# Performance work log

Measured on AMD Instinct MI355X. Metric: run time of the kernel, lower is better.

## Reference

```python
import jax, jax.numpy as jnp
import numpy as np

B, N, IN_F, E, H, A = 8, 1024, 1024, 256, 4, 64
ALPHA = 0.2          # leaky relu slope
NEG = -9e15          # mask value from original code


def setup_inputs() -> dict:
    key = jax.random.key(0)
    k = jax.random.split(key, 7)
    x = jax.random.normal(k[0], (B * N, IN_F), dtype=jnp.float32)
    adj = jax.random.randint(k[1], (B, N, N), 0, 2, dtype=jnp.int32)
    # per-head GAT params: W (H, IN_F, E); a split into a1, a2 (H, E) each,
    # since cat([Wh_i, Wh_j]) @ a == Wh_i @ a1 + Wh_j @ a2 exactly.
    W = jax.random.normal(k[2], (H, IN_F, E), dtype=jnp.float32) * 0.05
    a1 = jax.random.normal(k[3], (H, E), dtype=jnp.float32) * 0.05
    a2 = jax.random.normal(k[4], (H, E), dtype=jnp.float32) * 0.05
    W_act = jax.random.normal(k[5], (H * E, A), dtype=jnp.float32) * 0.05
    b_act = jnp.zeros((A,), dtype=jnp.float32)
    return {"x": x, "adj": adj, "W": W, "a1": a1, "a2": a2,
            "W_act": W_act, "b_act": b_act}


def reference(x, adj, W, a1, a2, W_act, b_act):
    b, n, _ = adj.shape
    xr = x.reshape(b, n, -1)                                   # (B, N, IN_F)
    Wh = jnp.einsum('bni,hio->hbno', xr, W)                    # (H, B, N, E)
    f1 = jnp.einsum('hbno,ho->hbn', Wh, a1)                    # a . Wh_i part
    f2 = jnp.einsum('hbno,ho->hbn', Wh, a2)                    # a . Wh_j part
    e = jax.nn.leaky_relu(f1[..., :, None] + f2[..., None, :], ALPHA)  # (H,B,N,N)
    e = jnp.where(adj[None] > 0, e, NEG)
    att = jax.nn.softmax(e, axis=-1)                           # masked softmax
    h_prime = jnp.einsum('hbnm,hbmo->hbno', att, Wh)           # (H, B, N, E)
    h_prime = jax.nn.elu(h_prime)                              # concat=True -> elu
    feat = jnp.transpose(h_prime, (1, 2, 0, 3)).reshape(b * n, H * E)
    return feat @ W_act + b_act                                # (B*N, A)
```

## Files before the change

### kernel.cpp

```cpp
#include <hip/hip_runtime.h>
#include <stdint.h>

typedef __attribute__((ext_vector_type(8))) short short8;
typedef __attribute__((ext_vector_type(4))) float f32x4;
typedef __attribute__((ext_vector_type(16))) float f32x16;


__device__ __forceinline__ float b2f(unsigned short u) {
    union { unsigned int i; float f; } v; v.i = ((unsigned int)u) << 16; return v.f;
}
__device__ __forceinline__ unsigned short f2b(float f) {
    union { float f; unsigned int i; } v; v.f = f;
    unsigned int u = v.i;
    u = (u + 0x7FFFu + ((u >> 16) & 1u)) >> 16;
    return (unsigned short)u;
}
__device__ __forceinline__ unsigned int cvtpk(float a, float b) {
    unsigned int r;
    asm("v_cvt_pk_bf16_f32 %0, %1, %2" : "=v"(r) : "v"(a), "v"(b));
    return r;
}
__device__ __forceinline__ float blo(unsigned int u) {
    union { unsigned int i; float f; } v; v.i = u << 16; return v.f;
}
__device__ __forceinline__ float bhi(unsigned int u) {
    union { unsigned int i; float f; } v; v.i = u & 0xFFFF0000u; return v.f;
}
__device__ __forceinline__ void glds16(const void* g, const void* l) {
    __builtin_amdgcn_global_load_lds(
        (const __attribute__((address_space(1))) unsigned int*)g,
        (__attribute__((address_space(3))) unsigned int*)l, 16, 0, 0);
}

__device__ __forceinline__ void cvt8(const void* in, unsigned short* out,
                                     int f, int grp) {
    if (f) {
        ((ushort4*)out)[grp * 2]     = ((const ushort4*)in)[grp * 2];
        ((ushort4*)out)[grp * 2 + 1] = ((const ushort4*)in)[grp * 2 + 1];
    } else {
        const float4* p = (const float4*)in + (size_t)grp * 2;
        float4 a = p[0], b = p[1];
        ushort4 o0, o1;
        o0.x = f2b(a.x); o0.y = f2b(a.y); o0.z = f2b(a.z); o0.w = f2b(a.w);
        o1.x = f2b(b.x); o1.y = f2b(b.y); o1.z = f2b(b.z); o1.w = f2b(b.w);
        ((ushort4*)out)[grp * 2]     = o0;
        ((ushort4*)out)[grp * 2 + 1] = o1;
    }
}

__global__ __launch_bounds__(256) void prep_all(
        const unsigned int* __restrict__ x4,
        const void* __restrict__ x, const void* __restrict__ W,
        const void* __restrict__ Wact,
        const void* __restrict__ a1, const void* __restrict__ a2,
        const void* __restrict__ bact,
        unsigned short* __restrict__ xb, unsigned short* __restrict__ WT,
        unsigned short* __restrict__ WactT,
        unsigned short* __restrict__ a1b, unsigned short* __restrict__ a2b,
        unsigned short* __restrict__ bactb,
        int* __restrict__ flag, float4* __restrict__ fz) {
    __shared__ unsigned int tile[64 * 65];
    __shared__ int sflag;
    int tid = threadIdx.x;
    int bid = blockIdx.x;
    if (bid >= 4352 && bid < 4416) {
        fz[(bid - 4352) * 256 + tid] = float4{0.f, 0.f, 0.f, 0.f};
        return;
    }
    if (tid < 64) {
        unsigned int wv = x4[tid];
        unsigned int e = (wv >> 7) & 0xFF;
        unsigned long long m = __ballot(e >= 100 && e <= 140);
        if (tid == 0) sflag = (__popcll(m) >= 48) ? 1 : 0;
    }
    __syncthreads();
    int f = sflag;

    if (bid < 4096) {
        cvt8(x, xb, f, bid * 256 + tid);
        return;
    }
    if (bid == 4416) {
        if (tid == 0) flag[0] = f;
        if (tid < 128) cvt8(a1, a1b, f, tid);
        else           cvt8(a2, a2b, f, tid - 128);
        if (tid < 8)   cvt8(bact, bactb, f, tid);
        return;
    }
    const void* in; unsigned short* out; int C, bt, c0, r0;
    if (bid < 4352) {
        int lb = bid - 4096;
        in = W; out = WT; C = 256;
        c0 = (lb & 3) * 64;
        r0 = ((lb >> 2) & 15) * 64;
        bt = lb >> 6;
    } else {
        int lb = bid - 4417;
        in = Wact; out = WactT; C = 64;
        c0 = 0; r0 = lb * 64; bt = 0;
    }
    int rl = tid >> 2;
    int cc = (tid & 3) * 16;
    size_t ibase = ((size_t)bt * 1024 + (r0 + rl)) * C + c0 + cc;
    unsigned short v[16];
    if (f) {
        const unsigned short* p = (const unsigned short*)in + ibase;
        short8 a = *(const short8*)p;
        short8 b = *(const short8*)(p + 8);
#pragma unroll
        for (int j = 0; j < 8; j++) { v[j] = (unsigned short)a[j]; v[8 + j] = (unsigned short)b[j]; }
    } else {
        const float* p = (const float*)in + ibase;
#pragma unroll
        for (int j = 0; j < 16; j++) v[j] = f2b(p[j]);
    }
#pragma unroll
    for (int j = 0; j < 16; j++)
        tile[(cc + j) * 65 + rl] = v[j];
    __syncthreads();
    int cl = tid >> 2;
    int rch = (tid & 3) * 16;
    unsigned short o[16];
#pragma unroll
    for (int j = 0; j < 16; j++)
        o[j] = (unsigned short)tile[cl * 65 + rch + j];
    unsigned short* op = out + ((size_t)bt * C + (c0 + cl)) * 1024 + r0 + rch;
#pragma unroll
    for (int q = 0; q < 4; q++) {
        ushort4 s; s.x = o[q*4]; s.y = o[q*4+1]; s.z = o[q*4+2]; s.w = o[q*4+3];
        ((ushort4*)op)[q] = s;
    }
}

__global__ void pack_adj(const int* __restrict__ adj,
                         unsigned int* __restrict__ maskT) {
    int gid = blockIdx.x * 256 + threadIdx.x;
    int lane = threadIdx.x & 63;
    unsigned long long m = __ballot(adj[gid] > 0);
    if (lane == 0) {
        int lin = gid >> 6;
        int mw = (lin & 15) * 2;
        int bn = lin >> 4;
        int b = bn >> 10, n = bn & 1023;
        maskT[(size_t)(b * 32 + mw) * 1024 + n]     = (unsigned int)m;
        maskT[(size_t)(b * 32 + mw + 1) * 1024 + n] = (unsigned int)(m >> 32);
    }
}

__global__ __launch_bounds__(256) void k1_gemm(
        const unsigned short* __restrict__ x,
        const unsigned short* __restrict__ WT,
        unsigned short* __restrict__ WhF,
        const unsigned short* __restrict__ a1b,
        const unsigned short* __restrict__ a2b,
        float* __restrict__ f1, float* __restrict__ f2) {
    __shared__ unsigned short smA[2][16 * 512];
    __shared__ unsigned short smB[2][16 * 512];
    int tid = threadIdx.x;
    int w = tid >> 6, lane = tid & 63;
    int lr = lane & 15, lq = lane >> 4;
    int lin = blockIdx.x + 8 * blockIdx.y;
    int xcd = lin & 7, kk = lin >> 3;
    int ct = kk >> 3;
    int rt = xcd * 8 + (kk & 7);
    int col0 = ct * 128;
    int row0 = rt * 128;
    int h = col0 >> 8;
    int e_base = col0 & 255;
    int b = row0 >> 10;
    int m_base = row0 & 1023;
    int wr = w >> 1, wc = w & 1;

    f32x4 acc[4][4] = {};

    auto stage = [&](int bb, int k0) {
#pragma unroll
        for (int s = 0; s < 4; s++) {
            int g = 4 * w + s;
            int rb = g & 7, kh = g >> 3;
            const unsigned short* srcA =
                x + (size_t)(row0 + rb * 16 + lr) * 1024 + k0 + kh * 32 + lq * 8;
            glds16(srcA, &smA[bb][g * 512]);
            const unsigned short* srcB =
                WT + (size_t)(h * 256 + e_base + rb * 16 + lr) * 1024
                   + k0 + kh * 32 + lq * 8;
            glds16(srcB, &smB[bb][g * 512]);
        }
    };

    stage(0, 0);
    __syncthreads();

    for (int t = 0; t < 16; t++) {
        int cur = t & 1;
        if (t < 15) stage(cur ^ 1, (t + 1) * 64);
#pragma unroll
        for (int kh = 0; kh < 2; kh++) {
            short8 af[4], bf[4];
#pragma unroll
            for (int i = 0; i < 4; i++)
                af[i] = *(const short8*)&smA[cur][(kh * 8 + wr * 4 + i) * 512 + lane * 8];
#pragma unroll
            for (int j = 0; j < 4; j++)
                bf[j] = *(const short8*)&smB[cur][(kh * 8 + wc * 4 + j) * 512 + lane * 8];
#pragma unroll
            for (int i = 0; i < 4; i++)
#pragma unroll
                for (int j = 0; j < 4; j++)
                    acc[i][j] = __builtin_amdgcn_mfma_f32_16x16x32_bf16(
                        af[i], bf[j], acc[i][j], 0, 0, 0);
        }
        __syncthreads();
    }

    int hb = h * 8 + b;
#pragma unroll
    for (int i = 0; i < 4; i++) {
#pragma unroll
        for (int j = 0; j < 4; j++) {
            int e = e_base + (wc * 4 + j) * 16 + lr;
            int et = e >> 5, e31 = e & 31;
            int m16 = (m_base >> 4) + wr * 4 + i;
            ushort4 vs;
            vs.x = f2b(acc[i][j][0]);
            vs.y = f2b(acc[i][j][1]);
            vs.z = f2b(acc[i][j][2]);
            vs.w = f2b(acc[i][j][3]);
            size_t idx = ((size_t)((hb * 8 + et) * 64 + m16) * 512)
                         + ((lq >> 1) * 32 + e31) * 8 + (lq & 1) * 4;
            *(ushort4*)&WhF[idx] = vs;
        }
    }

    const float LOG2E = 1.44269504f;
    float a1v[4], a2v[4];
#pragma unroll
    for (int j = 0; j < 4; j++) {
        int e = e_base + (wc * 4 + j) * 16 + lr;
        a1v[j] = b2f(a1b[h * 256 + e]);
        a2v[j] = b2f(a2b[h * 256 + e]);
    }
#pragma unroll
    for (int i = 0; i < 4; i++) {
#pragma unroll
        for (int reg = 0; reg < 4; reg++) {
            float s1 = 0.f, s2 = 0.f;
#pragma unroll
            for (int j = 0; j < 4; j++) {
                s1 += acc[i][j][reg] * a1v[j];
                s2 += acc[i][j][reg] * a2v[j];
            }
            s1 += __shfl_xor(s1, 1, 64); s2 += __shfl_xor(s2, 1, 64);
            s1 += __shfl_xor(s1, 2, 64); s2 += __shfl_xor(s2, 2, 64);
            s1 += __shfl_xor(s1, 4, 64); s2 += __shfl_xor(s2, 4, 64);
            s1 += __shfl_xor(s1, 8, 64); s2 += __shfl_xor(s2, 8, 64);
            if (lr == 0) {
                int m = m_base + (wr * 4 + i) * 16 + lq * 4 + reg;
                atomicAdd(&f1[hb * 1024 + m], s1 * LOG2E);
                atomicAdd(&f2[hb * 1024 + m], s2 * LOG2E);
            }
        }
    }
}

__global__ __launch_bounds__(512, 4) void k2_attn(
        const unsigned short* __restrict__ WhF,
        const unsigned int* __restrict__ maskT,
        const float* __restrict__ f1, const float* __restrict__ f2,
        unsigned short* __restrict__ feat) {
    __shared__ unsigned short ptile[2][2][32][40];
    __shared__ float dred[2][4][32];
    int tid = threadIdx.x;
    int w = tid >> 6, lane = tid & 63;
    int q = w & 3, wrg = w >> 2;
    int l5 = lane >> 5, l31 = lane & 31;
    int bid = blockIdx.x;
    int xcd = bid & 7, idx = bid >> 3;
    int hb = xcd + 8 * (idx >> 4);
    int rgb = idx & 15;
    int n0 = rgb * 64 + wrg * 32;
    int h = hb >> 3, b = hb & 7;
    int row = n0 + l31;
    float f1n = f1[hb * 1024 + row];
    const unsigned short* whb = WhF + (size_t)(hb * 8 + q * 2) * 64 * 512
                                + lane * 8;
    const unsigned int* mrow = maskT + (size_t)b * 32 * 1024 + row;
    const float* f2p = f2 + hb * 1024 + q * 8 + l5 * 4;
    int cshift = q * 8 + l5 * 4;

    f32x16 acc[2] = {};
    float den = 0.f;

    short8 bufA[2][2], bufB[2][2];
#pragma unroll
    for (int et = 0; et < 2; et++)
#pragma unroll
        for (int ks = 0; ks < 2; ks++)
            bufA[et][ks] = *(const short8*)(whb + (size_t)(et * 64 + ks) * 512);

    unsigned int mw = mrow[0];
    float4 fv = *(const float4*)f2p;

    for (int mb = 0; mb < 32; mb += 2) {
        {
            float fvv[4] = {fv.x, fv.y, fv.z, fv.w};
            unsigned int mloc = mw >> cshift;
            float pv[4];
#pragma unroll
            for (int j = 0; j < 4; j++) {
                float t_ = f1n + fvv[j];
                float e_ = fmaxf(t_, 0.2f * t_);
                pv[j] = ((mloc >> j) & 1u) ? exp2f(e_) : 0.f;
            }
            unsigned int r0 = cvtpk(pv[0], pv[1]);
            unsigned int r1 = cvtpk(pv[2], pv[3]);
            den += (blo(r0) + bhi(r0)) + (blo(r1) + bhi(r1));
            uint2 pr; pr.x = r0; pr.y = r1;
            *(uint2*)&ptile[0][wrg][l31][cshift] = pr;
            mw = mrow[(size_t)(mb + 1) * 1024];
            fv = *(const float4*)(f2p + (mb + 1) * 32);
            __syncthreads();
            short8 af0 = *(const short8*)&ptile[0][wrg][l31][l5 * 8];
            short8 af1 = *(const short8*)&ptile[0][wrg][l31][16 + l5 * 8];
            int m16n = (mb + 1) * 2;
#pragma unroll
            for (int et = 0; et < 2; et++)
#pragma unroll
                for (int ks = 0; ks < 2; ks++)
                    bufB[et][ks] =
                        *(const short8*)(whb + (size_t)(et * 64 + m16n + ks) * 512);
            __builtin_amdgcn_s_setprio(1);
#pragma unroll
            for (int et = 0; et < 2; et++) {
                acc[et] = __builtin_amdgcn_mfma_f32_32x32x16_bf16(
                    af0, bufA[et][0], acc[et], 0, 0, 0);
                acc[et] = __builtin_amdgcn_mfma_f32_32x32x16_bf16(
                    af1, bufA[et][1], acc[et], 0, 0, 0);
            }
            __builtin_amdgcn_s_setprio(0);
        }
        {
            float fvv[4] = {fv.x, fv.y, fv.z, fv.w};
            unsigned int mloc = mw >> cshift;
            float pv[4];
#pragma unroll
            for (int j = 0; j < 4; j++) {
                float t_ = f1n + fvv[j];
                float e_ = fmaxf(t_, 0.2f * t_);
                pv[j] = ((mloc >> j) & 1u) ? exp2f(e_) : 0.f;
            }
            unsigned int r0 = cvtpk(pv[0], pv[1]);
            unsigned int r1 = cvtpk(pv[2], pv[3]);
            den += (blo(r0) + bhi(r0)) + (blo(r1) + bhi(r1));
            uint2 pr; pr.x = r0; pr.y = r1;
            *(uint2*)&ptile[1][wrg][l31][cshift] = pr;
            if (mb < 30) {
                mw = mrow[(size_t)(mb + 2) * 1024];
                fv = *(const float4*)(f2p + (mb + 2) * 32);
            }
            __syncthreads();
            short8 af0 = *(const short8*)&ptile[1][wrg][l31][l5 * 8];
            short8 af1 = *(const short8*)&ptile[1][wrg][l31][16 + l5 * 8];
            if (mb < 30) {
                int m16n = (mb + 2) * 2;
#pragma unroll
                for (int et = 0; et < 2; et++)
#pragma unroll
                    for (int ks = 0; ks < 2; ks++)
                        bufA[et][ks] =
                            *(const short8*)(whb + (size_t)(et * 64 + m16n + ks) * 512);
            }
            __builtin_amdgcn_s_setprio(1);
#pragma unroll
            for (int et = 0; et < 2; et++) {
                acc[et] = __builtin_amdgcn_mfma_f32_32x32x16_bf16(
                    af0, bufB[et][0], acc[et], 0, 0, 0);
                acc[et] = __builtin_amdgcn_mfma_f32_32x32x16_bf16(
                    af1, bufB[et][1], acc[et], 0, 0, 0);
            }
            __builtin_amdgcn_s_setprio(0);
        }
    }

    den += __shfl_xor(den, 32, 64);
    if (l5 == 0) dred[wrg][q][l31] = den;
    __syncthreads();
    float denf = dred[wrg][0][l31] + dred[wrg][1][l31]
               + dred[wrg][2][l31] + dred[wrg][3][l31];

#pragma unroll
    for (int reg = 0; reg < 16; reg++) {
        int r = (reg & 3) + 8 * (reg >> 2) + 4 * l5;
        float dr = __shfl(denf, r, 64);
        float rdr = 1.0f / dr;
        int nn = n0 + r;
#pragma unroll
        for (int et = 0; et < 2; et++) {
            int e = q * 64 + et * 32 + l31;
            float v = acc[et][reg] * rdr;
            float o = v > 0.f ? v : __expf(v) - 1.f;
            feat[(size_t)(b * 1024 + nn) * 1024 + h * 256 + e] = f2b(o);
        }
    }
}

__global__ __launch_bounds__(256) void k3_out(
        const unsigned short* __restrict__ feat,
        const unsigned short* __restrict__ WactT,
        const unsigned short* __restrict__ bact,
        void* __restrict__ out, const int* __restrict__ flag) {
    __shared__ unsigned short smA[2][2 * 512];
    __shared__ unsigned short smB[2][4 * 512];
    int tid = threadIdx.x;
    int w = tid >> 6, lane = tid & 63;
    int lr = lane & 15, lq = lane >> 4;
    int row0 = blockIdx.x * 32;
    int g = w & 1, ch = w >> 1;
    int bf16out = *flag;
    f32x4 acc[2] = {};

    auto stage = [&](int bb, int k0) {
        if (w < 2) {
            const unsigned short* src =
                feat + (size_t)(row0 + w * 16 + lr) * 1024 + k0 + lq * 8;
            glds16(src, &smA[bb][w * 512]);
        } else {
#pragma unroll
            for (int s = 0; s < 2; s++) {
                int t = (w - 2) * 2 + s;
                const unsigned short* src =
                    WactT + (size_t)(t * 16 + lr) * 1024 + k0 + lq * 8;
                glds16(src, &smB[bb][t * 512]);
            }
        }
    };

    stage(0, 0);
    __syncthreads();

    for (int t = 0; t < 32; t++) {
        int cur = t & 1;
        if (t < 31) stage(cur ^ 1, (t + 1) * 32);
        short8 af = *(const short8*)&smA[cur][g * 512 + lane * 8];
#pragma unroll
        for (int j = 0; j < 2; j++) {
            short8 bf = *(const short8*)&smB[cur][(ch * 2 + j) * 512 + lane * 8];
            acc[j] = __builtin_amdgcn_mfma_f32_16x16x32_bf16(af, bf, acc[j], 0, 0, 0);
        }
        __syncthreads();
    }
#pragma unroll
    for (int j = 0; j < 2; j++) {
        int col = ch * 32 + j * 16 + lr;
        float bv = b2f(bact[col]);
#pragma unroll
        for (int rr = 0; rr < 4; rr++) {
            int r = row0 + g * 16 + lq * 4 + rr;
            float val = acc[j][rr] + bv;
            if (bf16out) ((unsigned short*)out)[(size_t)r * 64 + col] = f2b(val);
            else         ((float*)out)[(size_t)r * 64 + col] = val;
        }
    }
}

extern "C" void kernel_launch(void* const* d_in, const int* in_sizes, int n_in,
                              void* d_out, int out_size, void* d_ws, size_t ws_size,
                              hipStream_t stream) {
    const void* x    = d_in[0];
    const int*  adj  = (const int*)d_in[1];
    const void* W    = d_in[2];
    const void* a1   = d_in[3];
    const void* a2   = d_in[4];
    const void* Wact = d_in[5];
    const void* bact = d_in[6];

    char* ws = (char*)d_ws;
    unsigned short* WhF   = (unsigned short*)(ws);
    unsigned short* xb    = (unsigned short*)(ws + 16777216);
    unsigned short* feat  = (unsigned short*)(ws + 16777216);
    unsigned short* WT    = (unsigned short*)(ws + 33554432);
    unsigned int*   maskT = (unsigned int*)(ws + 33554432);
    unsigned short* WactT = (unsigned short*)(ws + 35651584);
    float*          f1    = (float*)(ws + 35782656);
    float*          f2    = (float*)(ws + 35913728);
    unsigned short* a1b   = (unsigned short*)(ws + 36044800);
    unsigned short* a2b   = (unsigned short*)(ws + 36046848);
    unsigned short* bactb = (unsigned short*)(ws + 36048896);
    int*            flag  = (int*)(ws + 36049024);
    if (ws_size < (size_t)36049040) return;

    prep_all<<<4433, 256, 0, stream>>>((const unsigned int*)x, x, W, Wact,
                                       a1, a2, bact, xb, WT, WactT,
                                       a1b, a2b, bactb, flag, (float4*)f1);
    k1_gemm<<<dim3(8, 64), 256, 0, stream>>>(xb, WT, WhF, a1b, a2b, f1, f2);
    pack_adj<<<32768, 256, 0, stream>>>(adj, maskT);
    k2_attn<<<512, 512, 0, stream>>>(WhF, maskT, f1, f2, feat);
    k3_out<<<256, 256, 0, stream>>>(feat, WactT, bactb, d_out, flag);
}
```

Before: 211.4 us.

## Halve k1 GEMM row tile and drop LDS double buffering for occupancy

The projection GEMM now uses 64x128 output tiles instead of 128x128, doubling the grid to 1024 blocks. The double-buffered LDS staging is replaced by a single buffer with sync-load-sync, which cuts shared memory to 24 KB per block, and launch bounds request 4 blocks per CU. The goal is more waves in flight and better CU fill so latency is hidden by occupancy rather than software pipelining. In exchange there is more B-tile reload traffic, less reuse per block, and the prefetch overlap is lost.

```diff
diff --git a/kernel.cpp b/kernel.cpp
--- a/kernel.cpp
+++ b/kernel.cpp
@@ -147,80 +147,78 @@
     }
 }
 
-__global__ __launch_bounds__(256) void k1_gemm(
+__global__ __launch_bounds__(256, 4) void k1_gemm(
         const unsigned short* __restrict__ x,
         const unsigned short* __restrict__ WT,
         unsigned short* __restrict__ WhF,
         const unsigned short* __restrict__ a1b,
         const unsigned short* __restrict__ a2b,
         float* __restrict__ f1, float* __restrict__ f2) {
-    __shared__ unsigned short smA[2][16 * 512];
-    __shared__ unsigned short smB[2][16 * 512];
+    __shared__ unsigned short smA[8 * 512];
+    __shared__ unsigned short smB[16 * 512];
     int tid = threadIdx.x;
     int w = tid >> 6, lane = tid & 63;
     int lr = lane & 15, lq = lane >> 4;
-    int lin = blockIdx.x + 8 * blockIdx.y;
+    int lin = blockIdx.x;
     int xcd = lin & 7, kk = lin >> 3;
-    int ct = kk >> 3;
-    int rt = xcd * 8 + (kk & 7);
+    int ct = kk >> 4;
+    int rt = xcd * 16 + (kk & 15);
     int col0 = ct * 128;
-    int row0 = rt * 128;
+    int row0 = rt * 64;
     int h = col0 >> 8;
     int e_base = col0 & 255;
     int b = row0 >> 10;
     int m_base = row0 & 1023;
     int wr = w >> 1, wc = w & 1;
 
-    f32x4 acc[4][4] = {};
-
-    auto stage = [&](int bb, int k0) {
-#pragma unroll
-        for (int s = 0; s < 4; s++) {
-            int g = 4 * w + s;
-            int rb = g & 7, kh = g >> 3;
-            const unsigned short* srcA =
-                x + (size_t)(row0 + rb * 16 + lr) * 1024 + k0 + kh * 32 + lq * 8;
-            glds16(srcA, &smA[bb][g * 512]);
-            const unsigned short* srcB =
-                WT + (size_t)(h * 256 + e_base + rb * 16 + lr) * 1024
-                   + k0 + kh * 32 + lq * 8;
-            glds16(srcB, &smB[bb][g * 512]);
-        }
-    };
-
-    stage(0, 0);
-    __syncthreads();
-
-    for (int t = 0; t < 16; t++) {
-        int cur = t & 1;
-        if (t < 15) stage(cur ^ 1, (t + 1) * 64);
+    f32x4 acc[2][4] = {};
+
+    for (int k0 = 0; k0 < 1024; k0 += 64) {
+        __syncthreads();
+#pragma unroll
+        for (int s = 0; s < 6; s++) {
+            int g = 6 * w + s;
+            if (g < 8) {
+                int rb = g & 3, kh = g >> 2;
+                const unsigned short* srcA =
+                    x + (size_t)(row0 + rb * 16 + lr) * 1024 + k0 + kh * 32 + lq * 8;
+                glds16(srcA, &smA[g * 512]);
+            } else {
+                int gb = g - 8;
+                int rb = gb & 7, kh = gb >> 3;
+                const unsigned short* srcB =
+                    WT + (size_t)(h * 256 + e_base + rb * 16 + lr) * 1024
+                       + k0 + kh * 32 + lq * 8;
+                glds16(srcB, &smB[gb * 512]);
+            }
+        }
+        __syncthreads();
 #pragma unroll
         for (int kh = 0; kh < 2; kh++) {
-            short8 af[4], bf[4];
-#pragma unroll
-            for (int i = 0; i < 4; i++)
-                af[i] = *(const short8*)&smA[cur][(kh * 8 + wr * 4 + i) * 512 + lane * 8];
+            short8 af[2], bf[4];
+#pragma unroll
+            for (int i = 0; i < 2; i++)
+                af[i] = *(const short8*)&smA[(kh * 4 + wr * 2 + i) * 512 + lane * 8];
 #pragma unroll
             for (int j = 0; j < 4; j++)
-                bf[j] = *(const short8*)&smB[cur][(kh * 8 + wc * 4 + j) * 512 + lane * 8];
-#pragma unroll
-            for (int i = 0; i < 4; i++)
+                bf[j] = *(const short8*)&smB[(kh * 8 + wc * 4 + j) * 512 + lane * 8];
+#pragma unroll
+            for (int i = 0; i < 2; i++)
 #pragma unroll
                 for (int j = 0; j < 4; j++)
                     acc[i][j] = __builtin_amdgcn_mfma_f32_16x16x32_bf16(
                         af[i], bf[j], acc[i][j], 0, 0, 0);
         }
-        __syncthreads();
     }
 
     int hb = h * 8 + b;
 #pragma unroll
-    for (int i = 0; i < 4; i++) {
+    for (int i = 0; i < 2; i++) {
 #pragma unroll
         for (int j = 0; j < 4; j++) {
             int e = e_base + (wc * 4 + j) * 16 + lr;
             int et = e >> 5, e31 = e & 31;
-            int m16 = (m_base >> 4) + wr * 4 + i;
+            int m16 = (m_base >> 4) + wr * 2 + i;
             ushort4 vs;
             vs.x = f2b(acc[i][j][0]);
             vs.y = f2b(acc[i][j][1]);
@@ -241,7 +239,7 @@
         a2v[j] = b2f(a2b[h * 256 + e]);
     }
 #pragma unroll
-    for (int i = 0; i < 4; i++) {
+    for (int i = 0; i < 2; i++) {
 #pragma unroll
         for (int reg = 0; reg < 4; reg++) {
             float s1 = 0.f, s2 = 0.f;
@@ -255,7 +253,7 @@
             s1 += __shfl_xor(s1, 4, 64); s2 += __shfl_xor(s2, 4, 64);
             s1 += __shfl_xor(s1, 8, 64); s2 += __shfl_xor(s2, 8, 64);
             if (lr == 0) {
-                int m = m_base + (wr * 4 + i) * 16 + lq * 4 + reg;
+                int m = m_base + (wr * 2 + i) * 16 + lq * 4 + reg;
                 atomicAdd(&f1[hb * 1024 + m], s1 * LOG2E);
                 atomicAdd(&f2[hb * 1024 + m], s2 * LOG2E);
             }
@@ -492,7 +490,7 @@
     prep_all<<<4433, 256, 0, stream>>>((const unsigned int*)x, x, W, Wact,
                                        a1, a2, bact, xb, WT, WactT,
                                        a1b, a2b, bactb, flag, (float4*)f1);
-    k1_gemm<<<dim3(8, 64), 256, 0, stream>>>(xb, WT, WhF, a1b, a2b, f1, f2);
+    k1_gemm<<<1024, 256, 0, stream>>>(xb, WT, WhF, a1b, a2b, f1, f2);
     pack_adj<<<32768, 256, 0, stream>>>(adj, maskT);
     k2_attn<<<512, 512, 0, stream>>>(WhF, maskT, f1, f2, feat);
     k3_out<<<256, 256, 0, stream>>>(feat, WactT, bactb, d_out, flag);
```

After: 220.2 us. +4.2%, slower.
